# Kernel tuning notes

Measured on AMD Instinct MI355X. Metric: run time of the kernel, lower is better.

The kernel has to match this reference:

```python
import jax, jax.numpy as jnp
import numpy as np

B, N, FIN, FOUT, H = 8, 1024, 256, 256, 4
D = FOUT // H  # head_dim = 64
LN_EPS = 1e-5
NEG_INF = -1e9


def setup_inputs() -> dict:
    key = jax.random.key(0)
    k_x, k_adj, k_w, k_a = jax.random.split(key, 4)
    x = jax.random.normal(k_x, (B, N, FIN), dtype=jnp.float32)
    # sparse binary adjacency with self-loops (dense mask, as the module expects)
    adj = (jax.random.uniform(k_adj, (B, N, N)) < 0.05).astype(jnp.float32)
    adj = jnp.maximum(adj, jnp.eye(N, dtype=jnp.float32)[None])
    W = jax.random.normal(k_w, (FIN, FOUT), dtype=jnp.float32) * 0.02
    gamma = jnp.ones((FOUT,), dtype=jnp.float32)
    beta = jnp.zeros((FOUT,), dtype=jnp.float32)
    a = jax.random.normal(k_a, (2 * D,), dtype=jnp.float32) * 0.02
    return {"x": x, "adj_matrix": adj, "W": W, "gamma": gamma, "beta": beta, "a": a}


def reference(x, adj_matrix, W, gamma, beta, a):
    # h = LayerNorm(x @ W)
    h = jnp.einsum("bnf,fo->bno", x, W)
    mu = jnp.mean(h, axis=-1, keepdims=True)
    var = jnp.mean(jnp.square(h - mu), axis=-1, keepdims=True)
    h = (h - mu) * jax.lax.rsqrt(var + LN_EPS) * gamma + beta
    h = h.reshape(B, N, H, D)
    # a^T [h_i ; h_j] == a_src . h_i + a_dst . h_j  (exact decomposition of the
    # concat+Linear(2D->1) attention score, avoiding the O(B*N^2*H*2D) concat)
    a_src, a_dst = a[:D], a[D:]
    e_i = jnp.einsum("bnhd,d->bnh", h, a_src)  # term for node i (query)
    e_j = jnp.einsum("bnhd,d->bnh", h, a_dst)  # term for node j (key)
    e = e_i[:, :, None, :] + e_j[:, None, :, :]  # [B, N_i, N_j, H]
    e = jnp.where(e > 0, e, 0.2 * e)  # LeakyReLU(0.2)
    e = jnp.where(adj_matrix[..., None] == 0, NEG_INF, e)
    alpha = jax.nn.softmax(e, axis=2)  # softmax over neighbors j
    # dropout is identity in eval/reference mode
    h_out = jnp.einsum("bijh,bjhd->bihd", alpha, h)
    return h_out.reshape(B, N, FOUT)
```

## Files before the change

### kernel.cpp

```cpp
#include <hip/hip_runtime.h>
#include <hip/hip_bf16.h>

#define BB 8
#define NN 1024
#define FIN 256
#define FOUT 256
#define NH 4
#define CAP 192

typedef short short8 __attribute__((ext_vector_type(8)));
typedef short short4v __attribute__((ext_vector_type(4)));
typedef float floatx4 __attribute__((ext_vector_type(4)));

__device__ __forceinline__ short f2bf(float f) {
    unsigned int u = __builtin_bit_cast(unsigned int, f);
    unsigned int r = (u + 0x7fffu + ((u >> 16) & 1u)) >> 16;
    return (short)r;
}
__device__ __forceinline__ float bf2f(unsigned short s) {
    return __builtin_bit_cast(float, (unsigned int)s << 16);
}

__global__ __launch_bounds__(256) void k_wt(const float* __restrict__ W,
                                            unsigned short* __restrict__ Wt) {
    __shared__ unsigned short ts[64][80];
    const int k0 = blockIdx.x * 64, n0 = blockIdx.y * 64;
    const int t = threadIdx.x;
#pragma unroll
    for (int q = 0; q < 4; ++q) {
        int lin = t + q * 256;
        int r = lin >> 4, c4 = lin & 15;
        float4 v = *(const float4*)&W[(size_t)(k0 + r) * FOUT + n0 + c4 * 4];
        ts[c4 * 4 + 0][r] = (unsigned short)f2bf(v.x);
        ts[c4 * 4 + 1][r] = (unsigned short)f2bf(v.y);
        ts[c4 * 4 + 2][r] = (unsigned short)f2bf(v.z);
        ts[c4 * 4 + 3][r] = (unsigned short)f2bf(v.w);
    }
    __syncthreads();
#pragma unroll
    for (int q = 0; q < 2; ++q) {
        int lin = t + q * 256;
        int row = lin >> 3, kg = lin & 7;
        short8 s = *(short8*)&ts[row][kg * 8];
        *(short8*)&Wt[(size_t)(n0 + row) * FIN + k0 + kg * 8] = s;
    }
}

__global__ __launch_bounds__(256) void k_gemm_ln(const float* __restrict__ x,
                                                 const unsigned short* __restrict__ Wt,
                                                 const float* __restrict__ gamma,
                                                 const float* __restrict__ beta,
                                                 const float* __restrict__ a,
                                                 unsigned short* __restrict__ hb,
                                                 float* __restrict__ e_src,
                                                 float* __restrict__ e_dst) {
    __shared__ unsigned short As[16 * 264];
    __shared__ float sumL[4][16], sqL[4][16];
    const int m0 = blockIdx.x * 16;
    const int t = threadIdx.x;
    const int w = t >> 6, lane = t & 63, quad = lane >> 4, l15 = lane & 15;

#pragma unroll
    for (int q = 0; q < 4; ++q) {
        int lin = t + q * 256;
        int row = lin >> 6, c4 = lin & 63;
        float4 v = *(const float4*)&x[(size_t)(m0 + row) * FIN + c4 * 4];
        short4v s;
        s.x = f2bf(v.x); s.y = f2bf(v.y); s.z = f2bf(v.z); s.w = f2bf(v.w);
        *(short4v*)&As[row * 264 + c4 * 4] = s;
    }
    __syncthreads();

    floatx4 acc[4];
#pragma unroll
    for (int nt = 0; nt < 4; ++nt) acc[nt] = (floatx4)0.f;

#pragma unroll
    for (int ks = 0; ks < 8; ++ks) {
        short8 af = *(short8*)&As[l15 * 264 + ks * 32 + quad * 8];
#pragma unroll
        for (int nt = 0; nt < 4; ++nt) {
            short8 bf = *(const short8*)&Wt[(size_t)((w * 4 + nt) * 16 + l15) * FIN + ks * 32 + quad * 8];
            acc[nt] = __builtin_amdgcn_mfma_f32_16x16x32_bf16(af, bf, acc[nt], 0, 0, 0);
        }
    }

    float rs[4], rq[4];
#pragma unroll
    for (int reg = 0; reg < 4; ++reg) {
        float s = 0.f, q2 = 0.f;
#pragma unroll
        for (int nt = 0; nt < 4; ++nt) { float v = acc[nt][reg]; s += v; q2 = fmaf(v, v, q2); }
#pragma unroll
        for (int off = 1; off < 16; off <<= 1) { s += __shfl_xor(s, off); q2 += __shfl_xor(q2, off); }
        rs[reg] = s; rq[reg] = q2;
    }
    if (l15 == 0) {
#pragma unroll
        for (int reg = 0; reg < 4; ++reg) {
            sumL[w][quad * 4 + reg] = rs[reg];
            sqL[w][quad * 4 + reg] = rq[reg];
        }
    }
    __syncthreads();

    float g[4], bt[4], as_[4], ad_[4];
#pragma unroll
    for (int nt = 0; nt < 4; ++nt) {
        int col = w * 64 + nt * 16 + l15;
        g[nt] = gamma[col]; bt[nt] = beta[col];
        int d = nt * 16 + l15;
        as_[nt] = a[d]; ad_[nt] = a[64 + d];
    }

    float pes[4], ped[4];
#pragma unroll
    for (int reg = 0; reg < 4; ++reg) {
        int row = quad * 4 + reg;
        float mean = (sumL[0][row] + sumL[1][row] + sumL[2][row] + sumL[3][row]) * (1.f / 256.f);
        float msq  = (sqL[0][row] + sqL[1][row] + sqL[2][row] + sqL[3][row]) * (1.f / 256.f);
        float inv = rsqrtf(msq - mean * mean + 1e-5f);
        float es = 0.f, ed = 0.f;
#pragma unroll
        for (int nt = 0; nt < 4; ++nt) {
            float hn = (acc[nt][reg] - mean) * inv * g[nt] + bt[nt];
            As[row * 264 + w * 64 + nt * 16 + l15] = (unsigned short)f2bf(hn);
            es = fmaf(hn, as_[nt], es);
            ed = fmaf(hn, ad_[nt], ed);
        }
        pes[reg] = es; ped[reg] = ed;
    }
#pragma unroll
    for (int reg = 0; reg < 4; ++reg) {
#pragma unroll
        for (int off = 1; off < 16; off <<= 1) {
            pes[reg] += __shfl_xor(pes[reg], off);
            ped[reg] += __shfl_xor(ped[reg], off);
        }
    }
    if (l15 == 0) {
#pragma unroll
        for (int reg = 0; reg < 4; ++reg) {
            int rowg = m0 + quad * 4 + reg;
            e_src[rowg * NH + w] = pes[reg];
            e_dst[rowg * NH + w] = ped[reg];
        }
    }
    __syncthreads();

#pragma unroll
    for (int q = 0; q < 2; ++q) {
        int lin = t + q * 256;
        int row = lin >> 5, cg = lin & 31;
        short8 s = *(short8*)&As[row * 264 + cg * 8];
        *(short8*)&hb[(size_t)(m0 + row) * FOUT + cg * 8] = s;
    }
}

__global__ __launch_bounds__(256) void k_attn(const unsigned short* __restrict__ hb,
                                              const float* __restrict__ adj,
                                              const float* __restrict__ e_src,
                                              const float* __restrict__ e_dst,
                                              float* __restrict__ out) {
    __shared__ int cnt;
    __shared__ int jlist[CAP];
    __shared__ float4 wsl[CAP];
    __shared__ float accs[4][4][64];
    __shared__ float Ss[4][64];

    const int b = blockIdx.y;
    const int i = blockIdx.x;
    const int t = threadIdx.x;
    const int lane = t & 63;
    const int w = t >> 6;
    const unsigned short* hp = hb + (size_t)b * NN * FOUT;
    const float* adjp = adj + ((size_t)b * NN + i) * NN;
    const float* edp  = e_dst + (size_t)b * NN * NH;
    const float4 esv = *(const float4*)&e_src[((size_t)b * NN + i) * NH];

    if (t == 0) cnt = 0;
    __syncthreads();

    float4 av = *(const float4*)&adjp[t * 4];
    float am[4] = {av.x, av.y, av.z, av.w};
#pragma unroll
    for (int q = 0; q < 4; ++q) {
        bool nz = (am[q] != 0.0f);
        unsigned long long mask = __ballot(nz);
        int basew = 0;
        if (lane == 0) basew = mask ? atomicAdd(&cnt, __popcll(mask)) : 0;
        basew = __shfl(basew, 0);
        if (nz) {
            int pos = basew + __popcll(mask & ((1ull << lane) - 1ull));
            int j = t * 4 + q;
            float4 ed = *(const float4*)&edp[(size_t)j * NH];
            float e0 = esv.x + ed.x, e1 = esv.y + ed.y, e2 = esv.z + ed.z, e3 = esv.w + ed.w;
            e0 = e0 > 0.f ? e0 : 0.2f * e0;
            e1 = e1 > 0.f ? e1 : 0.2f * e1;
            e2 = e2 > 0.f ? e2 : 0.2f * e2;
            e3 = e3 > 0.f ? e3 : 0.2f * e3;
            float4 w4;
            w4.x = __expf(e0); w4.y = __expf(e1); w4.z = __expf(e2); w4.w = __expf(e3);
            jlist[pos] = j;
            wsl[pos] = w4;
        }
    }
    __syncthreads();

    const int n = cnt;
    const int fg = lane;
    const int hh = fg >> 4;
    float4 acc = make_float4(0.f, 0.f, 0.f, 0.f);
    float S = 0.f;

    int idx = w;
    while (idx + 12 < n) {
        int jj[4]; float wv[4]; short4v hv[4];
#pragma unroll
        for (int q = 0; q < 4; ++q) {
            int p = idx + 4 * q;
            jj[q] = jlist[p];
            wv[q] = ((const float*)&wsl[p])[hh];
        }
#pragma unroll
        for (int q = 0; q < 4; ++q)
            hv[q] = *(const short4v*)&hp[(size_t)jj[q] * FOUT + fg * 4];
#pragma unroll
        for (int q = 0; q < 4; ++q) {
            acc.x = fmaf(wv[q], bf2f((unsigned short)hv[q].x), acc.x);
            acc.y = fmaf(wv[q], bf2f((unsigned short)hv[q].y), acc.y);
            acc.z = fmaf(wv[q], bf2f((unsigned short)hv[q].z), acc.z);
            acc.w = fmaf(wv[q], bf2f((unsigned short)hv[q].w), acc.w);
            S += wv[q];
        }
        idx += 16;
    }
    for (; idx < n; idx += 4) {
        int j = jlist[idx];
        float wv = ((const float*)&wsl[idx])[hh];
        short4v hv = *(const short4v*)&hp[(size_t)j * FOUT + fg * 4];
        acc.x = fmaf(wv, bf2f((unsigned short)hv.x), acc.x);
        acc.y = fmaf(wv, bf2f((unsigned short)hv.y), acc.y);
        acc.z = fmaf(wv, bf2f((unsigned short)hv.z), acc.z);
        acc.w = fmaf(wv, bf2f((unsigned short)hv.w), acc.w);
        S += wv;
    }

    accs[w][0][fg] = acc.x; accs[w][1][fg] = acc.y;
    accs[w][2][fg] = acc.z; accs[w][3][fg] = acc.w;
    Ss[w][fg] = S;
    __syncthreads();

    if (t < 64) {
        float4 o = make_float4(0.f, 0.f, 0.f, 0.f);
        float St = 0.f;
#pragma unroll
        for (int q = 0; q < 4; ++q) {
            o.x += accs[q][0][t]; o.y += accs[q][1][t];
            o.z += accs[q][2][t]; o.w += accs[q][3][t];
            St += Ss[q][t];
        }
        float inv = 1.0f / St;
        o.x *= inv; o.y *= inv; o.z *= inv; o.w *= inv;
        *(float4*)&out[((size_t)b * NN + i) * FOUT + t * 4] = o;
    }
}

extern "C" void kernel_launch(void* const* d_in, const int* in_sizes, int n_in,
                              void* d_out, int out_size, void* d_ws, size_t ws_size,
                              hipStream_t stream) {
    const float* x     = (const float*)d_in[0];
    const float* adj   = (const float*)d_in[1];
    const float* W     = (const float*)d_in[2];
    const float* gamma = (const float*)d_in[3];
    const float* beta  = (const float*)d_in[4];
    const float* a     = (const float*)d_in[5];
    float* out = (float*)d_out;

    unsigned short* Wt = (unsigned short*)d_ws;
    unsigned short* hb = Wt + (size_t)FIN * FOUT;
    float* e_src = (float*)(hb + (size_t)BB * NN * FOUT);
    float* e_dst = e_src + (size_t)BB * NN * NH;

    k_wt<<<dim3(4, 4), 256, 0, stream>>>(W, Wt);
    k_gemm_ln<<<dim3(512), 256, 0, stream>>>(x, Wt, gamma, beta, a, hb, e_src, e_dst);
    k_attn<<<dim3(NN, BB), 256, 0, stream>>>(hb, adj, e_src, e_dst, out);
}
```

Measured before the change: 122.3 us.

## Assign one attention row per wavefront instead of one per block

The attention kernel now gives each of the four wavefronts in a block its own query row, and launches a quarter as many blocks. Each wave compacts its own neighbour list with ballot and popcount into per-wave shared memory. This removes the shared atomic counter, all block barriers, and the cross-wave shared-memory reduction at the end. In exchange each wave walks its full neighbour list alone, so per-row latency grows while there are more rows in flight.

```diff
diff --git a/kernel.cpp b/kernel.cpp
--- a/kernel.cpp
+++ b/kernel.cpp
@@ -162,69 +162,70 @@
                                               const float* __restrict__ e_src,
                                               const float* __restrict__ e_dst,
                                               float* __restrict__ out) {
-    __shared__ int cnt;
-    __shared__ int jlist[CAP];
-    __shared__ float4 wsl[CAP];
-    __shared__ float accs[4][4][64];
-    __shared__ float Ss[4][64];
+    __shared__ int jlist[4][CAP];
+    __shared__ float4 wsl[4][CAP];
 
     const int b = blockIdx.y;
-    const int i = blockIdx.x;
     const int t = threadIdx.x;
     const int lane = t & 63;
     const int w = t >> 6;
+    const int i = blockIdx.x * 4 + w;
     const unsigned short* hp = hb + (size_t)b * NN * FOUT;
     const float* adjp = adj + ((size_t)b * NN + i) * NN;
     const float* edp  = e_dst + (size_t)b * NN * NH;
     const float4 esv = *(const float4*)&e_src[((size_t)b * NN + i) * NH];
 
-    if (t == 0) cnt = 0;
-    __syncthreads();
-
-    float4 av = *(const float4*)&adjp[t * 4];
-    float am[4] = {av.x, av.y, av.z, av.w};
-#pragma unroll
-    for (int q = 0; q < 4; ++q) {
-        bool nz = (am[q] != 0.0f);
-        unsigned long long mask = __ballot(nz);
-        int basew = 0;
-        if (lane == 0) basew = mask ? atomicAdd(&cnt, __popcll(mask)) : 0;
-        basew = __shfl(basew, 0);
-        if (nz) {
-            int pos = basew + __popcll(mask & ((1ull << lane) - 1ull));
-            int j = t * 4 + q;
-            float4 ed = *(const float4*)&edp[(size_t)j * NH];
-            float e0 = esv.x + ed.x, e1 = esv.y + ed.y, e2 = esv.z + ed.z, e3 = esv.w + ed.w;
-            e0 = e0 > 0.f ? e0 : 0.2f * e0;
-            e1 = e1 > 0.f ? e1 : 0.2f * e1;
-            e2 = e2 > 0.f ? e2 : 0.2f * e2;
-            e3 = e3 > 0.f ? e3 : 0.2f * e3;
-            float4 w4;
-            w4.x = __expf(e0); w4.y = __expf(e1); w4.z = __expf(e2); w4.w = __expf(e3);
-            jlist[pos] = j;
-            wsl[pos] = w4;
-        }
-    }
-    __syncthreads();
-
-    const int n = cnt;
-    const int fg = lane;
-    const int hh = fg >> 4;
+    int* jl = jlist[w];
+    float4* wl = wsl[w];
+
+    float4 av[4];
+#pragma unroll
+    for (int c = 0; c < 4; ++c)
+        av[c] = *(const float4*)&adjp[c * 256 + lane * 4];
+
+    int cnt = 0;
+#pragma unroll
+    for (int c = 0; c < 4; ++c) {
+        float am[4] = {av[c].x, av[c].y, av[c].z, av[c].w};
+#pragma unroll
+        for (int q = 0; q < 4; ++q) {
+            bool nz = (am[q] != 0.0f);
+            unsigned long long mask = __ballot(nz);
+            if (nz) {
+                int pos = cnt + __popcll(mask & ((1ull << lane) - 1ull));
+                int j = c * 256 + lane * 4 + q;
+                float4 ed = *(const float4*)&edp[(size_t)j * NH];
+                float e0 = esv.x + ed.x, e1 = esv.y + ed.y;
+                float e2 = esv.z + ed.z, e3 = esv.w + ed.w;
+                e0 = e0 > 0.f ? e0 : 0.2f * e0;
+                e1 = e1 > 0.f ? e1 : 0.2f * e1;
+                e2 = e2 > 0.f ? e2 : 0.2f * e2;
+                e3 = e3 > 0.f ? e3 : 0.2f * e3;
+                float4 w4;
+                w4.x = __expf(e0); w4.y = __expf(e1);
+                w4.z = __expf(e2); w4.w = __expf(e3);
+                jl[pos] = j;
+                wl[pos] = w4;
+            }
+            cnt += (int)__popcll(mask);
+        }
+    }
+
+    const int hh = lane >> 4;
     float4 acc = make_float4(0.f, 0.f, 0.f, 0.f);
     float S = 0.f;
 
-    int idx = w;
-    while (idx + 12 < n) {
+    int idx = 0;
+    for (; idx + 4 <= cnt; idx += 4) {
         int jj[4]; float wv[4]; short4v hv[4];
 #pragma unroll
         for (int q = 0; q < 4; ++q) {
-            int p = idx + 4 * q;
-            jj[q] = jlist[p];
-            wv[q] = ((const float*)&wsl[p])[hh];
+            jj[q] = jl[idx + q];
+            wv[q] = ((const float*)&wl[idx + q])[hh];
         }
 #pragma unroll
         for (int q = 0; q < 4; ++q)
-            hv[q] = *(const short4v*)&hp[(size_t)jj[q] * FOUT + fg * 4];
+            hv[q] = *(const short4v*)&hp[(size_t)jj[q] * FOUT + lane * 4];
 #pragma unroll
         for (int q = 0; q < 4; ++q) {
             acc.x = fmaf(wv[q], bf2f((unsigned short)hv[q].x), acc.x);
@@ -233,12 +234,11 @@
             acc.w = fmaf(wv[q], bf2f((unsigned short)hv[q].w), acc.w);
             S += wv[q];
         }
-        idx += 16;
-    }
-    for (; idx < n; idx += 4) {
-        int j = jlist[idx];
-        float wv = ((const float*)&wsl[idx])[hh];
-        short4v hv = *(const short4v*)&hp[(size_t)j * FOUT + fg * 4];
+    }
+    for (; idx < cnt; ++idx) {
+        int j = jl[idx];
+        float wv = ((const float*)&wl[idx])[hh];
+        short4v hv = *(const short4v*)&hp[(size_t)j * FOUT + lane * 4];
         acc.x = fmaf(wv, bf2f((unsigned short)hv.x), acc.x);
         acc.y = fmaf(wv, bf2f((unsigned short)hv.y), acc.y);
         acc.z = fmaf(wv, bf2f((unsigned short)hv.z), acc.z);
@@ -246,24 +246,10 @@
         S += wv;
     }
 
-    accs[w][0][fg] = acc.x; accs[w][1][fg] = acc.y;
-    accs[w][2][fg] = acc.z; accs[w][3][fg] = acc.w;
-    Ss[w][fg] = S;
-    __syncthreads();
-
-    if (t < 64) {
-        float4 o = make_float4(0.f, 0.f, 0.f, 0.f);
-        float St = 0.f;
-#pragma unroll
-        for (int q = 0; q < 4; ++q) {
-            o.x += accs[q][0][t]; o.y += accs[q][1][t];
-            o.z += accs[q][2][t]; o.w += accs[q][3][t];
-            St += Ss[q][t];
-        }
-        float inv = 1.0f / St;
-        o.x *= inv; o.y *= inv; o.z *= inv; o.w *= inv;
-        *(float4*)&out[((size_t)b * NN + i) * FOUT + t * 4] = o;
-    }
+    float inv = 1.0f / S;
+    float4 o;
+    o.x = acc.x * inv; o.y = acc.y * inv; o.z = acc.z * inv; o.w = acc.w * inv;
+    *(float4*)&out[((size_t)b * NN + i) * FOUT + lane * 4] = o;
 }
 
 extern "C" void kernel_launch(void* const* d_in, const int* in_sizes, int n_in,
@@ -284,5 +270,5 @@
 
     k_wt<<<dim3(4, 4), 256, 0, stream>>>(W, Wt);
     k_gemm_ln<<<dim3(512), 256, 0, stream>>>(x, Wt, gamma, beta, a, hb, e_src, e_dst);
-    k_attn<<<dim3(NN, BB), 256, 0, stream>>>(hb, adj, e_src, e_dst, out);
-}
+    k_attn<<<dim3(NN / 4, BB), 256, 0, stream>>>(hb, adj, e_src, e_dst, out);
+}
```

Result: no change. 120.4 us (-1.5%).
